# Performance work log

Hardware: AMD Instinct MI355X
Metric: run time of the kernel (lower is better)

The kernel has to match this reference:

```python
import jax, jax.numpy as jnp
import numpy as np

B, L, T = 256, 1024, 128


def setup_inputs() -> dict:
    key = jax.random.key(0)
    k1, k2, k3, k4 = jax.random.split(key, 4)
    inputs = jax.random.normal(k1, (B, L, T), dtype=jnp.float32)
    lengths = jax.random.randint(k2, (B,), 1, L + 1, dtype=jnp.int32)
    tags = jax.random.randint(k3, (B, L), 0, T, dtype=jnp.int32)
    # learned CRF transition matrix (random_normal_initializer default stddev=0.05)
    transition_params = jax.random.normal(k4, (T, T), dtype=jnp.float32) * 0.05
    return {"inputs": inputs, "lengths": lengths, "tags": tags,
            "transition_params": transition_params}


def _crf_decode(x, trans, lengths):
    """Viterbi decode. x: [B,L,T], trans: [T,T], lengths: [B] -> tags [B,L] int32."""
    Bx, Lx, Tx = x.shape

    def fwd_step(state, inp):
        x_t, t = inp  # x_t: [B,T]
        scores = state[:, :, None] + trans[None]          # [B, T_prev, T_cur]
        bp = jnp.argmax(scores, axis=1).astype(jnp.int32)  # [B,T]
        new_state = jnp.max(scores, axis=1) + x_t           # [B,T]
        m = (t < lengths)[:, None]
        state = jnp.where(m, new_state, state)
        bp = jnp.where(m, bp, 0)
        return state, bp

    init = x[:, 0]                                          # [B,T]
    xs = (jnp.swapaxes(x[:, 1:], 0, 1), jnp.arange(1, Lx))
    state, bps = jax.lax.scan(fwd_step, init, xs)           # bps: [L-1,B,T]
    bps = jnp.concatenate([jnp.zeros((1, Bx, Tx), jnp.int32), bps], axis=0)  # bp[0] unused
    last_tag = jnp.argmax(state, axis=-1).astype(jnp.int32)  # [B] tag at position length-1

    def bwd_step(carry, inp):
        bp_t, t = inp
        emit = jnp.where(t < lengths, carry, 0)             # tags beyond length -> 0
        prev = jnp.take_along_axis(bp_t, carry[:, None], axis=1)[:, 0]
        carry = jnp.where((t > 0) & (t < lengths), prev, carry)
        return carry, emit

    _, tags_rev = jax.lax.scan(bwd_step, last_tag, (bps[::-1], jnp.arange(Lx)[::-1]))
    return jnp.swapaxes(tags_rev[::-1], 0, 1)               # [B,L]


def reference(inputs, lengths, tags, transition_params):
    # Decoder.call: tfa.text.crf_decode(inputs, transition_params, lengths)[0]
    return _crf_decode(inputs, transition_params, lengths)
```

## Files before the change

### kernel.cpp

```cpp
#include <hip/hip_runtime.h>

#define BB 256
#define LL 1024
#define TT 128
#define NTH 512
#define CH 64
#define TTP 129

typedef unsigned long long ull;

__device__ __forceinline__ void lds_barrier() {
    asm volatile("s_waitcnt lgkmcnt(0)\n\ts_barrier" ::);
}

template<int CTRL>
__device__ __forceinline__ float dpp_f(float v) {
    int r = __builtin_amdgcn_update_dpp(__float_as_int(v), __float_as_int(v),
                                        CTRL, 0xF, 0xF, false);
    return __int_as_float(r);
}

#define SP(i) ((i) + (((i) >> 5) << 2))

struct FwdSmem {
    float st[2][144];
    unsigned char tags[LL];
};

__global__ __launch_bounds__(NTH)
void viterbi_ws_kernel(const float* __restrict__ x,
                       const int* __restrict__ lengths,
                       const float* __restrict__ trans,
                       int* __restrict__ out,
                       float* __restrict__ ws) {
    __shared__ FwdSmem sm;
    extern __shared__ float dyn[];
    float* tT = dyn;
    float* bm = dyn + TTP * TT;
    float* bx = bm + CH * TT;

    const int b   = blockIdx.x;
    const int tid = threadIdx.x;
    const int j   = tid >> 2;
    const int q   = tid & 3;

    int lenb = lengths[b];
    if (lenb < 1) lenb = 1;
    if (lenb > LL) lenb = LL;

    float tc[32];
    #pragma unroll
    for (int ii = 0; ii < 32; ++ii)
        tc[ii] = trans[(q * 32 + ii) * TT + j];

    {
        const int jj = tid & (TT - 1);
        const int qq = tid >> 7;
        #pragma unroll
        for (int ii = 0; ii < 32; ++ii) {
            int r = qq * 32 + ii;
            tT[jj * TTP + r] = trans[r * TT + jj];
        }
    }

    const float* xb  = x  + (size_t)b * LL * TT;
    float*       wsb = ws + (size_t)b * LL * TT;

    if (tid < TT) { float v = xb[tid]; sm.st[0][SP(tid)] = v; wsb[tid] = v; }

    float xv = 0.0f;
    if (q == 0 && lenb > 1) xv = xb[TT + j];
    lds_barrier();

    int p = 0;
    for (int t = 1; t < lenb; ++t) {
        float xn = 0.0f;
        if (q == 0) {
            int tn = (t + 1 < lenb) ? (t + 1) : (lenb - 1);
            xn = xb[tn * TT + j];
        }

        const float4* st4 = reinterpret_cast<const float4*>(&sm.st[p][q * 36]);
        float m0 = -3.4e38f, m1 = -3.4e38f, m2 = -3.4e38f, m3 = -3.4e38f;
        #pragma unroll
        for (int k = 0; k < 8; ++k) {
            float4 sv = st4[k];
            m0 = fmaxf(m0, sv.x + tc[4 * k + 0]);
            m1 = fmaxf(m1, sv.y + tc[4 * k + 1]);
            m2 = fmaxf(m2, sv.z + tc[4 * k + 2]);
            m3 = fmaxf(m3, sv.w + tc[4 * k + 3]);
        }
        float bb = fmaxf(fmaxf(m0, m1), fmaxf(m2, m3));
        bb = fmaxf(bb, dpp_f<0xB1>(bb));
        bb = fmaxf(bb, dpp_f<0x4E>(bb));

        if (q == 0) {
            wsb[t * TT + j] = bb;
            sm.st[p ^ 1][SP(j)] = bb + xv;
            xv = xn;
        }
        p ^= 1;
        lds_barrier();
    }

    __syncthreads();

    int c = 0; float mv = 0.0f;
    const int l = tid;
    if (tid < 64) {
        float s0 = sm.st[p][SP(l)], s1 = sm.st[p][SP(l + 64)];
        float mm = fmaxf(s0, s1);
        #pragma unroll
        for (int off = 1; off < 64; off <<= 1)
            mm = fmaxf(mm, __shfl_xor(mm, off));
        ull blo = __ballot(s0 == mm);
        if (blo) c = __ffsll(blo) - 1;
        else     c = 64 + __ffsll(__ballot(s1 == mm)) - 1;
        if (lenb > 1) mv = wsb[(lenb - 1) * TT + c];
    }

    int rhi = lenb - 2;
    while (rhi >= 0) {
        int r0 = rhi - (CH - 1); if (r0 < 0) r0 = 0;
        int nrows = rhi - r0 + 1;
        const float4* wm4 = reinterpret_cast<const float4*>(wsb + r0 * TT);
        const float4* wx4 = reinterpret_cast<const float4*>(xb  + r0 * TT);
        float4* bm4 = reinterpret_cast<float4*>(bm);
        float4* bx4 = reinterpret_cast<float4*>(bx);
        int n4 = nrows * (TT / 4);
        for (int i4 = tid; i4 < n4; i4 += NTH) {
            bm4[i4] = wm4[i4];
            float4 v = wx4[i4];
            if (r0 == 0 && i4 < TT / 4) { v.x = 0.f; v.y = 0.f; v.z = 0.f; v.w = 0.f; }
            bx4[i4] = v;
        }
        lds_barrier();
        if (tid < 64) {
            for (int t = r0 + nrows; t >= r0 + 1; --t) {
                int row = (t - 1 - r0) * TT;
                float slo = (bm[row + l]      + bx[row + l])      + tT[c * TTP + l];
                float shi = (bm[row + 64 + l] + bx[row + 64 + l]) + tT[c * TTP + 64 + l];
                ull blo = __ballot(slo == mv);
                int nc;
                if (blo) nc = __ffsll(blo) - 1;
                else     nc = 64 + __ffsll(__ballot(shi == mv)) - 1;
                if (l == 0) sm.tags[t] = (unsigned char)c;
                c = nc;
                mv = bm[row + c];
            }
        }
        lds_barrier();
        rhi = r0 - 1;
    }
    if (tid == 0) sm.tags[0] = (unsigned char)c;
    lds_barrier();

    int* outb = out + (size_t)b * LL;
    for (int t = tid; t < LL; t += NTH)
        outb[t] = (t < lenb) ? (int)sm.tags[t] : 0;
}

struct SmallSmem {
    float state[TT];
    float pv[NTH];
    int   pi[NTH];
    unsigned char tags[LL];
};

__global__ __launch_bounds__(NTH)
void viterbi_kernel(const float* __restrict__ x,
                    const int* __restrict__ lengths,
                    const float* __restrict__ trans,
                    int* __restrict__ out) {
    __shared__ SmallSmem sm;
    extern __shared__ unsigned char bp[];

    const int b   = blockIdx.x;
    const int tid = threadIdx.x;
    const int j   = tid & (TT - 1);
    const int q   = tid >> 7;

    int lenb = lengths[b];
    if (lenb < 1) lenb = 1;
    if (lenb > LL) lenb = LL;

    float tc[32];
    #pragma unroll
    for (int ii = 0; ii < 32; ++ii)
        tc[ii] = trans[(q * 32 + ii) * TT + j];

    const float* xb = x + (size_t)b * LL * TT;
    if (tid < TT) sm.state[tid] = xb[tid];

    float xv_cur = 0.0f, xv_next = 0.0f;
    if (tid < TT && lenb > 1) xv_cur = xb[TT + j];
    lds_barrier();

    for (int t = 1; t < lenb; ++t) {
        if (tid < TT) {
            int tn = (t + 1 < lenb) ? (t + 1) : (lenb - 1);
            xv_next = xb[tn * TT + j];
        }
        float best0 = -3.4e38f, best1 = -3.4e38f, best2 = -3.4e38f, best3 = -3.4e38f;
        int   bi0 = 0, bi1 = 1, bi2 = 2, bi3 = 3;
        const float4* st4 = reinterpret_cast<const float4*>(sm.state + q * 32);
        #pragma unroll
        for (int k = 0; k < 8; ++k) {
            float4 sv = st4[k];
            float s0 = sv.x + tc[4 * k + 0];
            float s1 = sv.y + tc[4 * k + 1];
            float s2 = sv.z + tc[4 * k + 2];
            float s3 = sv.w + tc[4 * k + 3];
            if (s0 > best0) { best0 = s0; bi0 = 4 * k + 0; }
            if (s1 > best1) { best1 = s1; bi1 = 4 * k + 1; }
            if (s2 > best2) { best2 = s2; bi2 = 4 * k + 2; }
            if (s3 > best3) { best3 = s3; bi3 = 4 * k + 3; }
        }
        float bb = best0; int bi = bi0;
        if (best1 > bb || (best1 == bb && bi1 < bi)) { bb = best1; bi = bi1; }
        if (best2 > bb || (best2 == bb && bi2 < bi)) { bb = best2; bi = bi2; }
        if (best3 > bb || (best3 == bb && bi3 < bi)) { bb = best3; bi = bi3; }
        sm.pv[tid] = bb;
        sm.pi[tid] = bi + q * 32;
        lds_barrier();

        if (tid < TT) {
            float bv = sm.pv[j];       int ix = sm.pi[j];
            float v1 = sm.pv[j + 128]; int i1 = sm.pi[j + 128];
            float v2 = sm.pv[j + 256]; int i2 = sm.pi[j + 256];
            float v3 = sm.pv[j + 384]; int i3 = sm.pi[j + 384];
            if (v1 > bv) { bv = v1; ix = i1; }
            if (v2 > bv) { bv = v2; ix = i2; }
            if (v3 > bv) { bv = v3; ix = i3; }
            sm.state[j] = bv + xv_cur;
            bp[t * TT + j] = (unsigned char)ix;
            xv_cur = xv_next;
        }
        lds_barrier();
    }

    if (tid == 0) {
        float bv = sm.state[0]; int ix = 0;
        for (int i = 1; i < TT; ++i) {
            float v = sm.state[i];
            if (v > bv) { bv = v; ix = i; }
        }
        int carry = ix;
        for (int t = lenb - 1; t >= 1; --t) {
            sm.tags[t] = (unsigned char)carry;
            carry = bp[t * TT + carry];
        }
        sm.tags[0] = (unsigned char)carry;
    }
    lds_barrier();

    int* outb = out + (size_t)b * LL;
    for (int t = tid; t < LL; t += NTH)
        outb[t] = (t < lenb) ? (int)sm.tags[t] : 0;
}

extern "C" void kernel_launch(void* const* d_in, const int* in_sizes, int n_in,
                              void* d_out, int out_size, void* d_ws, size_t ws_size,
                              hipStream_t stream) {
    const float* x       = (const float*)d_in[0];
    const int*   lengths = (const int*)d_in[1];
    const float* trans   = (const float*)d_in[3];
    int*         out     = (int*)d_out;

    const size_t ws_needed = (size_t)BB * LL * TT * sizeof(float);

    if (d_ws != nullptr && ws_size >= ws_needed) {
        const int dyn = (TTP * TT + 2 * CH * TT) * (int)sizeof(float);
        hipFuncSetAttribute((const void*)&viterbi_ws_kernel,
                            hipFuncAttributeMaxDynamicSharedMemorySize, dyn);
        viterbi_ws_kernel<<<BB, NTH, dyn, stream>>>(x, lengths, trans, out,
                                                    (float*)d_ws);
    } else {
        const int dyn = LL * TT;
        hipFuncSetAttribute((const void*)&viterbi_kernel,
                            hipFuncAttributeMaxDynamicSharedMemorySize, dyn);
        viterbi_kernel<<<BB, NTH, dyn, stream>>>(x, lengths, trans, out);
    }
}
```

Before: 825.8 us.

## Repartition Viterbi forward step by wavefront-owned previous tags with readlane broadcast

The forward max-plus recurrence is repartitioned so that each wavefront owns 16 previous tags and all 128 current tags. The previous-state values are broadcast into scalar registers via readlane instead of being read from LDS. Partial maxima per wave go to a double-buffered LDS array and are reduced across waves after one barrier. The final state is rebuilt from the workspace plus emissions, which removes the LDS state buffer. This trades the per-step LDS state reads for 16 readlanes plus a cross-wave partial-max exchange, and keeps one barrier per step.

```diff
diff --git a/kernel.cpp b/kernel.cpp
--- a/kernel.cpp
+++ b/kernel.cpp
@@ -6,6 +6,7 @@
 #define NTH 512
 #define CH 64
 #define TTP 129
+#define PVP 132
 
 typedef unsigned long long ull;
 
@@ -20,10 +21,8 @@
     return __int_as_float(r);
 }
 
-#define SP(i) ((i) + (((i) >> 5) << 2))
-
 struct FwdSmem {
-    float st[2][144];
+    float pv[2][8 * PVP];
     unsigned char tags[LL];
 };
 
@@ -41,17 +40,26 @@
 
     const int b   = blockIdx.x;
     const int tid = threadIdx.x;
-    const int j   = tid >> 2;
-    const int q   = tid & 3;
+    const int l   = tid & 63;
+    const int w   = tid >> 6;
+    const int il  = l >> 2;
+    const int k   = l & 3;
 
     int lenb = lengths[b];
     if (lenb < 1) lenb = 1;
     if (lenb > LL) lenb = LL;
 
-    float tc[32];
+    float tcA[16], tcB[16];
     #pragma unroll
-    for (int ii = 0; ii < 32; ++ii)
-        tc[ii] = trans[(q * 32 + ii) * TT + j];
+    for (int ii = 0; ii < 16; ++ii) {
+        tcA[ii] = trans[(w * 16 + ii) * TT + l];
+        tcB[ii] = trans[(w * 16 + ii) * TT + l + 64];
+    }
+    #pragma unroll
+    for (int ii = 0; ii < 16; ++ii) {
+        asm volatile("" : "+v"(tcA[ii]));
+        asm volatile("" : "+v"(tcB[ii]));
+    }
 
     {
         const int jj = tid & (TT - 1);
@@ -66,49 +74,69 @@
     const float* xb  = x  + (size_t)b * LL * TT;
     float*       wsb = ws + (size_t)b * LL * TT;
 
-    if (tid < TT) { float v = xb[tid]; sm.st[0][SP(tid)] = v; wsb[tid] = v; }
+    if (tid < TT) wsb[tid] = xb[tid];
+
+    float ssg[16];
+    {
+        float v0 = xb[w * 16 + il];
+        #pragma unroll
+        for (int ii = 0; ii < 16; ++ii)
+            ssg[ii] = __int_as_float(
+                __builtin_amdgcn_readlane(__float_as_int(v0), 4 * ii));
+    }
 
     float xv = 0.0f;
-    if (q == 0 && lenb > 1) xv = xb[TT + j];
-    lds_barrier();
-
-    int p = 0;
+    if (lenb > 1) xv = xb[TT + w * 16 + il];
+
     for (int t = 1; t < lenb; ++t) {
-        float xn = 0.0f;
-        if (q == 0) {
-            int tn = (t + 1 < lenb) ? (t + 1) : (lenb - 1);
-            xn = xb[tn * TT + j];
-        }
-
-        const float4* st4 = reinterpret_cast<const float4*>(&sm.st[p][q * 36]);
-        float m0 = -3.4e38f, m1 = -3.4e38f, m2 = -3.4e38f, m3 = -3.4e38f;
-        #pragma unroll
-        for (int k = 0; k < 8; ++k) {
-            float4 sv = st4[k];
-            m0 = fmaxf(m0, sv.x + tc[4 * k + 0]);
-            m1 = fmaxf(m1, sv.y + tc[4 * k + 1]);
-            m2 = fmaxf(m2, sv.z + tc[4 * k + 2]);
-            m3 = fmaxf(m3, sv.w + tc[4 * k + 3]);
-        }
-        float bb = fmaxf(fmaxf(m0, m1), fmaxf(m2, m3));
-        bb = fmaxf(bb, dpp_f<0xB1>(bb));
-        bb = fmaxf(bb, dpp_f<0x4E>(bb));
-
-        if (q == 0) {
-            wsb[t * TT + j] = bb;
-            sm.st[p ^ 1][SP(j)] = bb + xv;
-            xv = xn;
-        }
-        p ^= 1;
-        lds_barrier();
+        int tn = (t + 1 < lenb) ? (t + 1) : (lenb - 1);
+        float xn = xb[tn * TT + w * 16 + il];
+
+        float a0 = -3.4e38f, a1 = -3.4e38f, a2 = -3.4e38f, a3 = -3.4e38f;
+        float b0 = -3.4e38f, b1 = -3.4e38f, b2 = -3.4e38f, b3 = -3.4e38f;
+        #pragma unroll
+        for (int ii = 0; ii < 16; ii += 4) {
+            a0 = fmaxf(a0, ssg[ii + 0] + tcA[ii + 0]);
+            a1 = fmaxf(a1, ssg[ii + 1] + tcA[ii + 1]);
+            a2 = fmaxf(a2, ssg[ii + 2] + tcA[ii + 2]);
+            a3 = fmaxf(a3, ssg[ii + 3] + tcA[ii + 3]);
+            b0 = fmaxf(b0, ssg[ii + 0] + tcB[ii + 0]);
+            b1 = fmaxf(b1, ssg[ii + 1] + tcB[ii + 1]);
+            b2 = fmaxf(b2, ssg[ii + 2] + tcB[ii + 2]);
+            b3 = fmaxf(b3, ssg[ii + 3] + tcB[ii + 3]);
+        }
+        float* pvw = &sm.pv[t & 1][w * PVP];
+        pvw[l]      = fmaxf(fmaxf(a0, a1), fmaxf(a2, a3));
+        pvw[l + 64] = fmaxf(fmaxf(b0, b1), fmaxf(b2, b3));
+        lds_barrier();
+
+        const float* pvb = sm.pv[t & 1];
+        float va = pvb[(2 * k)     * PVP + w * 16 + il];
+        float vb = pvb[(2 * k + 1) * PVP + w * 16 + il];
+        float m = fmaxf(va, vb);
+        m = fmaxf(m, dpp_f<0xB1>(m));
+        m = fmaxf(m, dpp_f<0x4E>(m));
+        if (k == 0) wsb[t * TT + w * 16 + il] = m;
+        float sval = m + xv;
+        #pragma unroll
+        for (int ii = 0; ii < 16; ++ii)
+            ssg[ii] = __int_as_float(
+                __builtin_amdgcn_readlane(__float_as_int(sval), 4 * ii));
+        xv = xn;
     }
 
     __syncthreads();
 
     int c = 0; float mv = 0.0f;
-    const int l = tid;
     if (tid < 64) {
-        float s0 = sm.st[p][SP(l)], s1 = sm.st[p][SP(l + 64)];
+        const float* mrow = wsb + (size_t)(lenb - 1) * TT;
+        float s0, s1;
+        if (lenb > 1) {
+            s0 = mrow[l]      + xb[(lenb - 1) * TT + l];
+            s1 = mrow[l + 64] + xb[(lenb - 1) * TT + l + 64];
+        } else {
+            s0 = mrow[l]; s1 = mrow[l + 64];
+        }
         float mm = fmaxf(s0, s1);
         #pragma unroll
         for (int off = 1; off < 64; off <<= 1)
@@ -116,7 +144,7 @@
         ull blo = __ballot(s0 == mm);
         if (blo) c = __ffsll(blo) - 1;
         else     c = 64 + __ffsll(__ballot(s1 == mm)) - 1;
-        if (lenb > 1) mv = wsb[(lenb - 1) * TT + c];
+        if (lenb > 1) mv = mrow[c];
     }
 
     int rhi = lenb - 2;
@@ -136,15 +164,15 @@
         }
         lds_barrier();
         if (tid < 64) {
-            for (int t = r0 + nrows; t >= r0 + 1; --t) {
-                int row = (t - 1 - r0) * TT;
+            for (int tt = r0 + nrows; tt >= r0 + 1; --tt) {
+                int row = (tt - 1 - r0) * TT;
                 float slo = (bm[row + l]      + bx[row + l])      + tT[c * TTP + l];
                 float shi = (bm[row + 64 + l] + bx[row + 64 + l]) + tT[c * TTP + 64 + l];
                 ull blo = __ballot(slo == mv);
                 int nc;
                 if (blo) nc = __ffsll(blo) - 1;
                 else     nc = 64 + __ffsll(__ballot(shi == mv)) - 1;
-                if (l == 0) sm.tags[t] = (unsigned char)c;
+                if (l == 0) sm.tags[tt] = (unsigned char)c;
                 c = nc;
                 mv = bm[row + c];
             }
@@ -156,8 +184,8 @@
     lds_barrier();
 
     int* outb = out + (size_t)b * LL;
-    for (int t = tid; t < LL; t += NTH)
-        outb[t] = (t < lenb) ? (int)sm.tags[t] : 0;
+    for (int tt = tid; tt < LL; tt += NTH)
+        outb[tt] = (tt < lenb) ? (int)sm.tags[tt] : 0;
 }
 
 struct SmallSmem {
@@ -205,16 +233,16 @@
         int   bi0 = 0, bi1 = 1, bi2 = 2, bi3 = 3;
         const float4* st4 = reinterpret_cast<const float4*>(sm.state + q * 32);
         #pragma unroll
-        for (int k = 0; k < 8; ++k) {
-            float4 sv = st4[k];
-            float s0 = sv.x + tc[4 * k + 0];
-            float s1 = sv.y + tc[4 * k + 1];
-            float s2 = sv.z + tc[4 * k + 2];
-            float s3 = sv.w + tc[4 * k + 3];
-            if (s0 > best0) { best0 = s0; bi0 = 4 * k + 0; }
-            if (s1 > best1) { best1 = s1; bi1 = 4 * k + 1; }
-            if (s2 > best2) { best2 = s2; bi2 = 4 * k + 2; }
-            if (s3 > best3) { best3 = s3; bi3 = 4 * k + 3; }
+        for (int kk = 0; kk < 8; ++kk) {
+            float4 sv = st4[kk];
+            float s0 = sv.x + tc[4 * kk + 0];
+            float s1 = sv.y + tc[4 * kk + 1];
+            float s2 = sv.z + tc[4 * kk + 2];
+            float s3 = sv.w + tc[4 * kk + 3];
+            if (s0 > best0) { best0 = s0; bi0 = 4 * kk + 0; }
+            if (s1 > best1) { best1 = s1; bi1 = 4 * kk + 1; }
+            if (s2 > best2) { best2 = s2; bi2 = 4 * kk + 2; }
+            if (s3 > best3) { best3 = s3; bi3 = 4 * kk + 3; }
         }
         float bb = best0; int bi = bi0;
         if (best1 > bb || (best1 == bb && bi1 < bi)) { bb = best1; bi = bi1; }
```

Result: slower. 868.3 us (+5.2%).
